# Kernel tuning notes

Hardware: AMD Instinct MI355X
Metric: run time of the kernel (lower is better)

Reference implementation:

```python
import jax, jax.numpy as jnp
import numpy as np

COST_CLASS = 2.0
COST_BBOX = 5.0
COST_GIOU = 2.0
NUM_ORGANS = 20


def _cxcyczwhd_to_xyzxyz(b):
    c, s = b[..., :3], b[..., 3:]
    return jnp.concatenate([c - 0.5 * s, c + 0.5 * s], axis=-1)


def _giou3d(a, b):
    # a, b: [..., 6] xyzxyz, elementwise-paired (b broadcasts)
    vol_a = jnp.prod(a[..., 3:] - a[..., :3], axis=-1)
    vol_b = jnp.prod(b[..., 3:] - b[..., :3], axis=-1)
    lt = jnp.maximum(a[..., :3], b[..., :3])
    rb = jnp.minimum(a[..., 3:], b[..., 3:])
    inter = jnp.prod(jnp.clip(rb - lt, 0.0), axis=-1)
    union = vol_a + vol_b - inter
    iou = inter / union
    lt_c = jnp.minimum(a[..., :3], b[..., :3])
    rb_c = jnp.maximum(a[..., 3:], b[..., 3:])
    vol_c = jnp.prod(jnp.clip(rb_c - lt_c, 0.0), axis=-1)
    return iou - (vol_c - union) / vol_c


def setup_inputs() -> dict:
    key = jax.random.key(0)
    k1, k2, k3, k4, k5 = jax.random.split(key, 5)
    bs, O, Qp = 16, NUM_ORGANS, 8192
    nq = O * Qp
    pred_logits = jax.random.normal(k1, (bs, nq, 1), dtype=jnp.float32)
    pred_boxes = jax.random.uniform(k2, (bs, nq, 6), dtype=jnp.float32)
    anchors = jax.random.uniform(k3, (nq, 6), dtype=jnp.float32)
    # targets: centers in [0,1], sizes in [0.05, 0.3]
    tb_c = jax.random.uniform(k4, (bs, O, 3), dtype=jnp.float32)
    tb_s = 0.05 + 0.25 * jax.random.uniform(jax.random.fold_in(k4, 1), (bs, O, 3), dtype=jnp.float32)
    target_boxes = jnp.concatenate([tb_c, tb_s], axis=-1)
    target_present = jax.random.randint(k5, (bs, O), 0, 2, dtype=jnp.int32)
    return {
        'pred_logits': pred_logits,
        'pred_boxes': pred_boxes,
        'anchors': anchors,
        'target_boxes': target_boxes,
        'target_present': target_present,
        'num_top_queries': 1,
    }


def reference(pred_logits, pred_boxes, anchors, target_boxes, target_present, num_top_queries):
    bs, nq, _ = pred_logits.shape
    O = target_boxes.shape[1]
    Qp = nq // O
    # anchor_matching=True: boxes come from anchors, broadcast over batch
    boxes = jnp.broadcast_to(anchors[None], (bs, nq, 6)).reshape(bs, O, Qp, 6)
    logits = pred_logits.reshape(bs, O, Qp)
    tgt = target_boxes[:, :, None, :]  # [bs, O, 1, 6]

    cost_class = -jax.nn.sigmoid(logits)                      # [bs, O, Qp]
    cost_bbox = jnp.abs(boxes - tgt).sum(-1)                  # L1 cdist to single target
    cost_giou = -_giou3d(_cxcyczwhd_to_xyzxyz(jnp.clip(boxes, 0.0)),
                         _cxcyczwhd_to_xyzxyz(tgt))           # [bs, O, Qp]
    C = COST_BBOX * cost_bbox + COST_CLASS * cost_class + COST_GIOU * cost_giou

    # top-k smallest cost queries per (batch, organ)
    _, best_ids = jax.lax.top_k(-C, num_top_queries)          # [bs, O, k]
    present = target_present.astype(bool)                     # [bs, O]
    matches = jnp.clip(jax.nn.one_hot(best_ids, Qp, dtype=jnp.int32).sum(-2), 0, 1)
    matches = matches * present[..., None].astype(jnp.int32)  # absent class -> all zeros

    cg_max = cost_giou.max(-1, keepdims=True)
    cg_min = cost_giou.min(-1, keepdims=True)
    sl = jnp.clip((cost_giou - cg_max) / (cg_min - cg_max), 0.0)
    soft_labels = jnp.where(present[..., None], sl, -1.0)
    return matches, soft_labels
```

## Files before the change

### kernel.cpp

```cpp
#include <hip/hip_runtime.h>
#include <math.h>

#define NUM_O 20
#define QP    8192
#define NT    512
#define PER   (QP / NT)

__global__ __launch_bounds__(NT) void matcher_kernel(
    const float* __restrict__ pred_logits,
    const float* __restrict__ anchors,
    const float* __restrict__ target_boxes,
    const int*   __restrict__ target_present,
    float* __restrict__ out_matches,
    float* __restrict__ out_soft)
{
    const int bo  = blockIdx.x;
    const int b   = bo / NUM_O;
    const int o   = bo % NUM_O;
    const int tid = threadIdx.x;

    const float* t = target_boxes + (size_t)bo * 6;
    const float t0 = t[0], t1 = t[1], t2 = t[2], t3 = t[3], t4 = t[4], t5 = t[5];
    const float tlo0 = t0 - 0.5f * t3, tlo1 = t1 - 0.5f * t4, tlo2 = t2 - 0.5f * t5;
    const float thi0 = t0 + 0.5f * t3, thi1 = t1 + 0.5f * t4, thi2 = t2 + 0.5f * t5;
    const float vol_b = ((thi0 - tlo0) * (thi1 - tlo1)) * (thi2 - tlo2);

    const float* anc = anchors + (size_t)o * QP * 6;
    const float* lg  = pred_logits + ((size_t)b * NUM_O + o) * QP;

    float cg[PER];
    float bestC  = INFINITY;
    int   bestIdx = 0x7fffffff;
    float cgmin = INFINITY, cgmax = -INFINITY;

    #pragma unroll
    for (int i = 0; i < PER; i++) {
        const int q = tid + i * NT;
        const float* a = anc + (size_t)q * 6;
        const float2 a01 = *(const float2*)(a);
        const float2 a23 = *(const float2*)(a + 2);
        const float2 a45 = *(const float2*)(a + 4);
        const float ax = a01.x, ay = a01.y, az = a23.x;
        const float aw = a23.y, ah = a45.x, ad = a45.y;

        float cbox = fabsf(ax - t0);
        cbox += fabsf(ay - t1);
        cbox += fabsf(az - t2);
        cbox += fabsf(aw - t3);
        cbox += fabsf(ah - t4);
        cbox += fabsf(ad - t5);

        const float cx = fmaxf(ax, 0.0f), cy = fmaxf(ay, 0.0f), cz = fmaxf(az, 0.0f);
        const float cw = fmaxf(aw, 0.0f), chh = fmaxf(ah, 0.0f), cd = fmaxf(ad, 0.0f);
        const float alo0 = cx - 0.5f * cw,  alo1 = cy - 0.5f * chh, alo2 = cz - 0.5f * cd;
        const float ahi0 = cx + 0.5f * cw,  ahi1 = cy + 0.5f * chh, ahi2 = cz + 0.5f * cd;
        const float vol_a = ((ahi0 - alo0) * (ahi1 - alo1)) * (ahi2 - alo2);

        const float lt0 = fmaxf(alo0, tlo0), lt1 = fmaxf(alo1, tlo1), lt2 = fmaxf(alo2, tlo2);
        const float rb0 = fminf(ahi0, thi0), rb1 = fminf(ahi1, thi1), rb2 = fminf(ahi2, thi2);
        const float i0 = fmaxf(rb0 - lt0, 0.0f), i1 = fmaxf(rb1 - lt1, 0.0f), i2 = fmaxf(rb2 - lt2, 0.0f);
        const float inter = (i0 * i1) * i2;
        const float uni   = vol_a + vol_b - inter;
        const float iou   = inter / uni;

        const float clo0 = fminf(alo0, tlo0), clo1 = fminf(alo1, tlo1), clo2 = fminf(alo2, tlo2);
        const float chi0 = fmaxf(ahi0, thi0), chi1 = fmaxf(ahi1, thi1), chi2 = fmaxf(ahi2, thi2);
        const float e0 = fmaxf(chi0 - clo0, 0.0f), e1 = fmaxf(chi1 - clo1, 0.0f), e2 = fmaxf(chi2 - clo2, 0.0f);
        const float vol_c = (e0 * e1) * e2;
        const float giou  = iou - (vol_c - uni) / vol_c;
        const float cgv   = -giou;

        const float logit = lg[q];
        const float sig   = 1.0f / (1.0f + expf(-logit));
        const float cc    = -sig;

        float C = 5.0f * cbox + 2.0f * cc;
        C = C + 2.0f * cgv;

        cg[i] = cgv;
        cgmin = fminf(cgmin, cgv);
        cgmax = fmaxf(cgmax, cgv);
        if (C < bestC) { bestC = C; bestIdx = q; }
        else if (C == bestC && q < bestIdx) { bestIdx = q; }
    }

    #pragma unroll
    for (int off = 32; off > 0; off >>= 1) {
        const float oc = __shfl_down(bestC, off);
        const int   oi = __shfl_down(bestIdx, off);
        if (oc < bestC || (oc == bestC && oi < bestIdx)) { bestC = oc; bestIdx = oi; }
        cgmin = fminf(cgmin, __shfl_down(cgmin, off));
        cgmax = fmaxf(cgmax, __shfl_down(cgmax, off));
    }

    __shared__ float s_c[NT / 64], s_mn[NT / 64], s_mx[NT / 64];
    __shared__ int   s_i[NT / 64];
    __shared__ float sh_mx, sh_den;
    __shared__ int   sh_best;
    const int wave = tid >> 6;
    if ((tid & 63) == 0) { s_c[wave] = bestC; s_i[wave] = bestIdx; s_mn[wave] = cgmin; s_mx[wave] = cgmax; }
    __syncthreads();
    if (tid == 0) {
        float bc = s_c[0]; int bi = s_i[0];
        float mn = s_mn[0], mx = s_mx[0];
        #pragma unroll
        for (int w = 1; w < NT / 64; w++) {
            if (s_c[w] < bc || (s_c[w] == bc && s_i[w] < bi)) { bc = s_c[w]; bi = s_i[w]; }
            mn = fminf(mn, s_mn[w]);
            mx = fmaxf(mx, s_mx[w]);
        }
        sh_best = bi;
        sh_mx   = mx;
        sh_den  = mn - mx;
    }
    __syncthreads();

    const int   best = sh_best;
    const float mx   = sh_mx;
    const float den  = sh_den;
    const bool  present = (target_present[bo] != 0);

    float* om = out_matches + (size_t)bo * QP;
    float* os = out_soft    + (size_t)bo * QP;

    #pragma unroll
    for (int i = 0; i < PER; i++) {
        const int q = tid + i * NT;
        om[q] = (present && q == best) ? 1.0f : 0.0f;
        float sl;
        if (present) {
            sl = fmaxf((cg[i] - mx) / den, 0.0f);
        } else {
            sl = -1.0f;
        }
        os[q] = sl;
    }
}

extern "C" void kernel_launch(void* const* d_in, const int* in_sizes, int n_in,
                              void* d_out, int out_size, void* d_ws, size_t ws_size,
                              hipStream_t stream) {
    const float* pred_logits   = (const float*)d_in[0];
    const float* anchors       = (const float*)d_in[2];
    const float* target_boxes  = (const float*)d_in[3];
    const int*   target_present = (const int*)d_in[4];

    const int nq = in_sizes[2] / 6;
    const int bs = in_sizes[0] / nq;

    float* out_matches = (float*)d_out;
    float* out_soft    = out_matches + (size_t)bs * nq;

    matcher_kernel<<<bs * NUM_O, NT, 0, stream>>>(
        pred_logits, anchors, target_boxes, target_present, out_matches, out_soft);
}
```

Measured before the change: 127.8 us.

## Split per-organ matcher into two kernels with more blocks and vectorized loads

Replaces the single kernel that used one block per (batch, organ) with two kernels. The first splits each row across 8 blocks, writes cost_giou and per-split partial argmin/min/max to workspace. The second reduces the partials and writes the outputs with float4 stores. Each thread now handles 4 contiguous queries using float4 loads. The aim is to raise parallelism beyond 320 blocks on a large GPU and to coalesce the loads. The cost is a workspace round-trip for cost_giou and an extra kernel launch.

```diff
diff --git a/kernel.cpp b/kernel.cpp
--- a/kernel.cpp
+++ b/kernel.cpp
@@ -1,20 +1,25 @@
 #include <hip/hip_runtime.h>
 #include <math.h>
 
-#define NUM_O 20
-#define QP    8192
-#define NT    512
-#define PER   (QP / NT)
+#define NUM_O   20
+#define QP      8192
+#define SPLITS  8
+#define NT1     256
+#define PER1    (QP / SPLITS / NT1)
+#define NT2     256
+#define BO_TOT  (16 * NUM_O)
 
-__global__ __launch_bounds__(NT) void matcher_kernel(
+
+__global__ __launch_bounds__(NT1) void matcher_phase1(
     const float* __restrict__ pred_logits,
     const float* __restrict__ anchors,
     const float* __restrict__ target_boxes,
-    const int*   __restrict__ target_present,
-    float* __restrict__ out_matches,
-    float* __restrict__ out_soft)
+    float* __restrict__ ws_cg,
+    float4* __restrict__ ws_part)
 {
-    const int bo  = blockIdx.x;
+    const int id  = blockIdx.x;
+    const int bo  = id >> 3;
+    const int s   = id & 7;
     const int b   = bo / NUM_O;
     const int o   = bo % NUM_O;
     const int tid = threadIdx.x;
@@ -25,23 +30,29 @@
     const float thi0 = t0 + 0.5f * t3, thi1 = t1 + 0.5f * t4, thi2 = t2 + 0.5f * t5;
     const float vol_b = ((thi0 - tlo0) * (thi1 - tlo1)) * (thi2 - tlo2);
 
-    const float* anc = anchors + (size_t)o * QP * 6;
-    const float* lg  = pred_logits + ((size_t)b * NUM_O + o) * QP;
+    const int q0 = s * (QP / SPLITS) + tid * PER1;
+    const float* anc = anchors + (size_t)o * QP * 6 + (size_t)q0 * 6;
+    const float* lg  = pred_logits + ((size_t)b * NUM_O + o) * QP + q0;
 
-    float cg[PER];
-    float bestC  = INFINITY;
+    float arr[24];
+    #pragma unroll
+    for (int k = 0; k < 6; k++) {
+        const float4 v = ((const float4*)anc)[k];
+        arr[4 * k + 0] = v.x; arr[4 * k + 1] = v.y;
+        arr[4 * k + 2] = v.z; arr[4 * k + 3] = v.w;
+    }
+    const float4 lgv = *(const float4*)lg;
+    const float logits4[4] = { lgv.x, lgv.y, lgv.z, lgv.w };
+
+    float cg4[PER1];
+    float bestC = INFINITY;
     int   bestIdx = 0x7fffffff;
     float cgmin = INFINITY, cgmax = -INFINITY;
 
     #pragma unroll
-    for (int i = 0; i < PER; i++) {
-        const int q = tid + i * NT;
-        const float* a = anc + (size_t)q * 6;
-        const float2 a01 = *(const float2*)(a);
-        const float2 a23 = *(const float2*)(a + 2);
-        const float2 a45 = *(const float2*)(a + 4);
-        const float ax = a01.x, ay = a01.y, az = a23.x;
-        const float aw = a23.y, ah = a45.x, ad = a45.y;
+    for (int j = 0; j < PER1; j++) {
+        const float ax = arr[6 * j + 0], ay = arr[6 * j + 1], az = arr[6 * j + 2];
+        const float aw = arr[6 * j + 3], ah = arr[6 * j + 4], ad = arr[6 * j + 5];
 
         float cbox = fabsf(ax - t0);
         cbox += fabsf(ay - t1);
@@ -70,19 +81,18 @@
         const float giou  = iou - (vol_c - uni) / vol_c;
         const float cgv   = -giou;
 
-        const float logit = lg[q];
-        const float sig   = 1.0f / (1.0f + expf(-logit));
-        const float cc    = -sig;
-
-        float C = 5.0f * cbox + 2.0f * cc;
+        const float sig = 1.0f / (1.0f + expf(-logits4[j]));
+        float C = 5.0f * cbox + 2.0f * (-sig);
         C = C + 2.0f * cgv;
 
-        cg[i] = cgv;
+        cg4[j] = cgv;
         cgmin = fminf(cgmin, cgv);
         cgmax = fmaxf(cgmax, cgv);
+        const int q = q0 + j;
         if (C < bestC) { bestC = C; bestIdx = q; }
-        else if (C == bestC && q < bestIdx) { bestIdx = q; }
     }
+
+    *(float4*)(ws_cg + (size_t)bo * QP + q0) = make_float4(cg4[0], cg4[1], cg4[2], cg4[3]);
 
     #pragma unroll
     for (int off = 32; off > 0; off >>= 1) {
@@ -93,10 +103,8 @@
         cgmax = fmaxf(cgmax, __shfl_down(cgmax, off));
     }
 
-    __shared__ float s_c[NT / 64], s_mn[NT / 64], s_mx[NT / 64];
-    __shared__ int   s_i[NT / 64];
-    __shared__ float sh_mx, sh_den;
-    __shared__ int   sh_best;
+    __shared__ float s_c[NT1 / 64], s_mn[NT1 / 64], s_mx[NT1 / 64];
+    __shared__ int   s_i[NT1 / 64];
     const int wave = tid >> 6;
     if ((tid & 63) == 0) { s_c[wave] = bestC; s_i[wave] = bestIdx; s_mn[wave] = cgmin; s_mx[wave] = cgmax; }
     __syncthreads();
@@ -104,45 +112,64 @@
         float bc = s_c[0]; int bi = s_i[0];
         float mn = s_mn[0], mx = s_mx[0];
         #pragma unroll
-        for (int w = 1; w < NT / 64; w++) {
+        for (int w = 1; w < NT1 / 64; w++) {
             if (s_c[w] < bc || (s_c[w] == bc && s_i[w] < bi)) { bc = s_c[w]; bi = s_i[w]; }
             mn = fminf(mn, s_mn[w]);
             mx = fmaxf(mx, s_mx[w]);
         }
-        sh_best = bi;
-        sh_mx   = mx;
-        sh_den  = mn - mx;
+        ws_part[id] = make_float4(bc, __int_as_float(bi), mn, mx);
     }
-    __syncthreads();
+}
 
-    const int   best = sh_best;
-    const float mx   = sh_mx;
-    const float den  = sh_den;
-    const bool  present = (target_present[bo] != 0);
+__global__ __launch_bounds__(NT2) void matcher_phase2(
+    const float4* __restrict__ ws_part,
+    const float* __restrict__ ws_cg,
+    const int*   __restrict__ target_present,
+    float* __restrict__ out_matches,
+    float* __restrict__ out_soft)
+{
+    const int id  = blockIdx.x;
+    const int bo  = id >> 3;
+    const int s   = id & 7;
+    const int tid = threadIdx.x;
 
-    float* om = out_matches + (size_t)bo * QP;
-    float* os = out_soft    + (size_t)bo * QP;
+    const float4* p = ws_part + (size_t)bo * SPLITS;
+    float bc = INFINITY; int bi = 0x7fffffff;
+    float mn = INFINITY, mx = -INFINITY;
+    #pragma unroll
+    for (int w = 0; w < SPLITS; w++) {
+        const float4 v = p[w];
+        const float c = v.x; const int i = __float_as_int(v.y);
+        if (c < bc || (c == bc && i < bi)) { bc = c; bi = i; }
+        mn = fminf(mn, v.z);
+        mx = fmaxf(mx, v.w);
+    }
+    const float den = mn - mx;
+    const bool present = (target_present[bo] != 0);
 
+    const int q0 = s * (QP / SPLITS) + tid * 4;
+    const float4 cgv = *(const float4*)(ws_cg + (size_t)bo * QP + q0);
+    const float cg4[4] = { cgv.x, cgv.y, cgv.z, cgv.w };
+
+    float4 m, sl;
+    float* mp = (float*)&m;
+    float* sp = (float*)&sl;
     #pragma unroll
-    for (int i = 0; i < PER; i++) {
-        const int q = tid + i * NT;
-        om[q] = (present && q == best) ? 1.0f : 0.0f;
-        float sl;
-        if (present) {
-            sl = fmaxf((cg[i] - mx) / den, 0.0f);
-        } else {
-            sl = -1.0f;
-        }
-        os[q] = sl;
+    for (int j = 0; j < 4; j++) {
+        const int q = q0 + j;
+        mp[j] = (present && q == bi) ? 1.0f : 0.0f;
+        sp[j] = present ? fmaxf((cg4[j] - mx) / den, 0.0f) : -1.0f;
     }
+    *(float4*)(out_matches + (size_t)bo * QP + q0) = m;
+    *(float4*)(out_soft    + (size_t)bo * QP + q0) = sl;
 }
 
 extern "C" void kernel_launch(void* const* d_in, const int* in_sizes, int n_in,
                               void* d_out, int out_size, void* d_ws, size_t ws_size,
                               hipStream_t stream) {
-    const float* pred_logits   = (const float*)d_in[0];
-    const float* anchors       = (const float*)d_in[2];
-    const float* target_boxes  = (const float*)d_in[3];
+    const float* pred_logits    = (const float*)d_in[0];
+    const float* anchors        = (const float*)d_in[2];
+    const float* target_boxes   = (const float*)d_in[3];
     const int*   target_present = (const int*)d_in[4];
 
     const int nq = in_sizes[2] / 6;
@@ -151,6 +178,12 @@
     float* out_matches = (float*)d_out;
     float* out_soft    = out_matches + (size_t)bs * nq;
 
-    matcher_kernel<<<bs * NUM_O, NT, 0, stream>>>(
-        pred_logits, anchors, target_boxes, target_present, out_matches, out_soft);
+    float*  ws_cg   = (float*)d_ws;
+    float4* ws_part = (float4*)((char*)d_ws + (size_t)bs * nq * 4);
+
+    const int nblk = bs * NUM_O * SPLITS;
+    matcher_phase1<<<nblk, NT1, 0, stream>>>(pred_logits, anchors, target_boxes,
+                                             ws_cg, ws_part);
+    matcher_phase2<<<nblk, NT2, 0, stream>>>(ws_part, ws_cg, target_present,
+                                             out_matches, out_soft);
 }
```

Measured after the change: 121.8 us. 1.05x faster.
